# Optimization experiments

Hardware: AMD Instinct MI355X
Metric: run time of the kernel (lower is better)

## Reference

```python
import jax, jax.numpy as jnp
import numpy as np

K = 8        # fused SOS sections
C = 64       # channels (B*C after reshape)
T = 262144   # time samples (~6 s @ 44.1 kHz)


def setup_inputs() -> dict:
    key = jax.random.key(0)
    kx, kb, ka1, ka2 = jax.random.split(key, 4)
    x = jax.random.normal(kx, (C, T), dtype=jnp.float32)
    # Stable biquad coefficients: a0 = 1, |a1| < 0.5, |a2| < 0.4 keeps poles
    # strictly inside the unit circle (|a1| < 1 + a2 and |a2| < 1).
    b = jax.random.normal(kb, (K, 3), dtype=jnp.float32) * 0.3
    a1 = jax.random.uniform(ka1, (K, 1), minval=-0.5, maxval=0.5, dtype=jnp.float32)
    a2 = jax.random.uniform(ka2, (K, 1), minval=-0.4, maxval=0.4, dtype=jnp.float32)
    sos = jnp.concatenate([b, jnp.ones((K, 1), jnp.float32), a1, a2], axis=1)
    state_x = jnp.zeros((K, C, 2), jnp.float32)  # [x[n-1], x[n-2]] per section/channel
    state_y = jnp.zeros((K, C, 2), jnp.float32)  # [y[n-1], y[n-2]]
    return {"x": x, "sos": sos, "state_x": state_x, "state_y": state_y}


def _biquad_df1(x, b0, b1, b2, a1, a2, sx, sy):
    """Direct-form-1 biquad over time, vectorized across channels.

    x: [C, T]; sx, sy: [C, 2] holding (lag1, lag2). Returns y: [C, T].
    """
    def step(carry, xn):
        x1, x2, y1, y2 = carry
        yn = b0 * xn + b1 * x1 + b2 * x2 - a1 * y1 - a2 * y2
        return (xn, x1, yn, y1), yn

    init = (sx[:, 0], sx[:, 1], sy[:, 0], sy[:, 1])
    _, ys = jax.lax.scan(step, init, x.T)  # scan over T, carry [C]
    return ys.T


def reference(x, sos, state_x, state_y):
    # Serial cascade of K second-order sections (fallback path of forward()).
    out = x
    k = sos.shape[0]
    for s in range(k):
        out = _biquad_df1(out, sos[s, 0], sos[s, 1], sos[s, 2],
                          sos[s, 4], sos[s, 5], state_x[s], state_y[s])
    return out
```

## Files before the change

### kernel.cpp

```cpp
#include <hip/hip_runtime.h>

#define C 64
#define T 262144
#define K 8
#define L 256
#define W 192
#define B (T / L)
#define TT 64
#define OSTRIDE 65
#define TMAX (T - 16)

#define STEP(Y1, Y2, U1, U2, XIN)                                            \
  {                                                                          \
    float tkv[K];                                                            \
    tkv[0] = fmaf(b1c[0], U1,                                                \
             fmaf(b2c[0], U2, fmaf(na1[0], Y1[0], na2[0] * Y2[0])));         \
    _Pragma("unroll")                                                        \
    for (int k = 1; k < K; ++k)                                              \
      tkv[k] = fmaf(b1c[k], Y1[k - 1],                                       \
               fmaf(b2c[k], Y2[k - 1],                                       \
               fmaf(na1[k], Y1[k], na2[k] * Y2[k])));                        \
    float o = fmaf(b0c[0], (XIN), tkv[0]);                                   \
    U2 = (XIN);                                                              \
    _Pragma("unroll")                                                        \
    for (int k = 1; k < K; ++k) {                                            \
      float o2 = fmaf(b0c[k], o, tkv[k]);                                    \
      Y2[k - 1] = o;                                                         \
      o = o2;                                                                \
    }                                                                        \
    Y2[K - 1] = o;                                                           \
    lastout = o;                                                             \
  }

#define GROUP(XS, CBASE)                                                     \
  _Pragma("unroll")                                                          \
  for (int j = 0; j < 16; j += 2) {                                          \
    STEP(yA, yB, uA, uB, XS[j])                                              \
    orow[(CBASE) + j] = lastout;                                             \
    STEP(yB, yA, uB, uA, XS[j + 1])                                          \
    orow[(CBASE) + j + 1] = lastout;                                         \
  }

#define LOAD16(DST, PTR)                                                     \
  {                                                                          \
    const float4* p4_ = (const float4*)(PTR);                                \
    float4 q0_ = p4_[0], q1_ = p4_[1], q2_ = p4_[2], q3_ = p4_[3];           \
    DST[0] = q0_.x;  DST[1] = q0_.y;  DST[2] = q0_.z;  DST[3] = q0_.w;       \
    DST[4] = q1_.x;  DST[5] = q1_.y;  DST[6] = q1_.z;  DST[7] = q1_.w;       \
    DST[8] = q2_.x;  DST[9] = q2_.y;  DST[10] = q2_.z; DST[11] = q2_.w;      \
    DST[12] = q3_.x; DST[13] = q3_.y; DST[14] = q3_.z; DST[15] = q3_.w;      \
  }

__global__ __launch_bounds__(64) void sos_kernel(
    const float* __restrict__ x, const float* __restrict__ sos,
    const float* __restrict__ sx, const float* __restrict__ sy,
    float* __restrict__ out) {
  __shared__ float obuf[64 * OSTRIDE];

  const int h = blockIdx.x;
  const int b = (h & 7) * (B / 8) + (h >> 3);
  const int lane = threadIdx.x;

  float b0c[K], b1c[K], b2c[K], na1[K], na2[K];
#pragma unroll
  for (int k = 0; k < K; ++k) {
    b0c[k] = sos[k * 6 + 0];
    b1c[k] = sos[k * 6 + 1];
    b2c[k] = sos[k * 6 + 2];
    na1[k] = -sos[k * 6 + 4];
    na2[k] = -sos[k * 6 + 5];
  }

  const int t_out = b * L;
  const int tstart = (t_out >= W) ? (t_out - W) : 0;
  const int nch = (t_out + L - tstart) / TT;

  const float* xrow = x + (size_t)lane * T;
  float* orow = &obuf[lane * OSTRIDE];

  float yA[K], yB[K], uA, uB;
  if (tstart == 0) {
    uA = sx[lane * 2 + 0];
    uB = sx[lane * 2 + 1];
#pragma unroll
    for (int k = 0; k < K; ++k) {
      yA[k] = sy[(k * 64 + lane) * 2 + 0];
      yB[k] = sy[(k * 64 + lane) * 2 + 1];
    }
  } else {
    uA = xrow[tstart - 1];
    uB = xrow[tstart - 2];
#pragma unroll
    for (int k = 0; k < K; ++k) { yA[k] = 0.f; yB[k] = 0.f; }
  }

  float xA[16], xB[16], xC[16], xD[16];
  LOAD16(xA, xrow + tstart)
  LOAD16(xB, xrow + tstart + 16)

  float lastout = 0.f;
  for (int ch = 0; ch < nch; ++ch) {
    const int tc = tstart + ch * TT;

    LOAD16(xC, xrow + tc + 32)
    GROUP(xA, 0)
    LOAD16(xD, xrow + tc + 48)
    GROUP(xB, 16)
    { int tl = tc + 64;  if (tl > TMAX) tl = TMAX;
      LOAD16(xA, xrow + tl) }
    GROUP(xC, 32)
    { int tl = tc + 80;  if (tl > TMAX) tl = TMAX;
      LOAD16(xB, xrow + tl) }
    GROUP(xD, 48)

    if (tc >= t_out) {
      const int rr = lane >> 4;
      const int cc = (lane & 15) * 4;
#pragma unroll
      for (int it = 0; it < 16; ++it) {
        const int r = it * 4 + rr;
        float4 v;
        v.x = obuf[r * OSTRIDE + cc + 0];
        v.y = obuf[r * OSTRIDE + cc + 1];
        v.z = obuf[r * OSTRIDE + cc + 2];
        v.w = obuf[r * OSTRIDE + cc + 3];
        *reinterpret_cast<float4*>(&out[(size_t)r * T + tc + cc]) = v;
      }
    }
  }
  (void)lastout;
}

extern "C" void kernel_launch(void* const* d_in, const int* in_sizes, int n_in,
                              void* d_out, int out_size, void* d_ws,
                              size_t ws_size, hipStream_t stream) {
  const float* x = (const float*)d_in[0];
  const float* sos = (const float*)d_in[1];
  const float* sx = (const float*)d_in[2];
  const float* sy = (const float*)d_in[3];
  float* out = (float*)d_out;
  (void)d_ws;

  sos_kernel<<<B, 64, 0, stream>>>(x, sos, sx, sy, out);
}
```

Measured before the change: 137.1 us.

## Double-buffer full 64-sample chunks in registers to prefetch a whole chunk ahead

Replaces the rolling four-slice prefetch with two full register chunk buffers (p and q) that alternate, issuing all loads for the next 64-sample chunk before computing the current one, with a sched_barrier to keep them ordered. The loop is unrolled by two to swap buffers without copies. Launch bounds now request one wave per SIMD so the compiler may use more registers. The aim is to hide more global load latency behind the serial recurrence, at the cost of higher register pressure.

```diff
diff --git a/kernel.cpp b/kernel.cpp
--- a/kernel.cpp
+++ b/kernel.cpp
@@ -51,7 +51,39 @@
     DST[12] = q3_.x; DST[13] = q3_.y; DST[14] = q3_.z; DST[15] = q3_.w;      \
   }
 
-__global__ __launch_bounds__(64) void sos_kernel(
+#define PART(C0, C1, C2, C3, N0, N1, N2, N3, TC)                             \
+  {                                                                          \
+    const int tc_ = (TC);                                                    \
+    int t0_ = tc_ + 64;  if (t0_ > TMAX) t0_ = TMAX;                         \
+    int t1_ = tc_ + 80;  if (t1_ > TMAX) t1_ = TMAX;                         \
+    int t2_ = tc_ + 96;  if (t2_ > TMAX) t2_ = TMAX;                         \
+    int t3_ = tc_ + 112; if (t3_ > TMAX) t3_ = TMAX;                         \
+    LOAD16(N0, xrow + t0_)                                                   \
+    LOAD16(N1, xrow + t1_)                                                   \
+    LOAD16(N2, xrow + t2_)                                                   \
+    LOAD16(N3, xrow + t3_)                                                   \
+    __builtin_amdgcn_sched_barrier(0);                                       \
+    GROUP(C0, 0)                                                             \
+    GROUP(C1, 16)                                                            \
+    GROUP(C2, 32)                                                            \
+    GROUP(C3, 48)                                                            \
+    if (tc_ >= t_out) {                                                      \
+      const int rr = lane >> 4;                                              \
+      const int cc = (lane & 15) * 4;                                        \
+      _Pragma("unroll")                                                      \
+      for (int it = 0; it < 16; ++it) {                                      \
+        const int r = it * 4 + rr;                                           \
+        float4 v;                                                            \
+        v.x = obuf[r * OSTRIDE + cc + 0];                                    \
+        v.y = obuf[r * OSTRIDE + cc + 1];                                    \
+        v.z = obuf[r * OSTRIDE + cc + 2];                                    \
+        v.w = obuf[r * OSTRIDE + cc + 3];                                    \
+        *reinterpret_cast<float4*>(&out[(size_t)r * T + tc_ + cc]) = v;      \
+      }                                                                      \
+    }                                                                        \
+  }
+
+__global__ __launch_bounds__(64, 1) void sos_kernel(
     const float* __restrict__ x, const float* __restrict__ sos,
     const float* __restrict__ sx, const float* __restrict__ sy,
     float* __restrict__ out) {
@@ -94,38 +126,19 @@
     for (int k = 0; k < K; ++k) { yA[k] = 0.f; yB[k] = 0.f; }
   }
 
-  float xA[16], xB[16], xC[16], xD[16];
-  LOAD16(xA, xrow + tstart)
-  LOAD16(xB, xrow + tstart + 16)
+  float pA[16], pB[16], pC[16], pD[16];
+  float qA[16], qB[16], qC[16], qD[16];
+  LOAD16(pA, xrow + tstart)
+  LOAD16(pB, xrow + tstart + 16)
+  LOAD16(pC, xrow + tstart + 32)
+  LOAD16(pD, xrow + tstart + 48)
 
   float lastout = 0.f;
-  for (int ch = 0; ch < nch; ++ch) {
+  for (int ch = 0; ch < nch; ch += 2) {
     const int tc = tstart + ch * TT;
-
-    LOAD16(xC, xrow + tc + 32)
-    GROUP(xA, 0)
-    LOAD16(xD, xrow + tc + 48)
-    GROUP(xB, 16)
-    { int tl = tc + 64;  if (tl > TMAX) tl = TMAX;
-      LOAD16(xA, xrow + tl) }
-    GROUP(xC, 32)
-    { int tl = tc + 80;  if (tl > TMAX) tl = TMAX;
-      LOAD16(xB, xrow + tl) }
-    GROUP(xD, 48)
-
-    if (tc >= t_out) {
-      const int rr = lane >> 4;
-      const int cc = (lane & 15) * 4;
-#pragma unroll
-      for (int it = 0; it < 16; ++it) {
-        const int r = it * 4 + rr;
-        float4 v;
-        v.x = obuf[r * OSTRIDE + cc + 0];
-        v.y = obuf[r * OSTRIDE + cc + 1];
-        v.z = obuf[r * OSTRIDE + cc + 2];
-        v.w = obuf[r * OSTRIDE + cc + 3];
-        *reinterpret_cast<float4*>(&out[(size_t)r * T + tc + cc]) = v;
-      }
+    PART(pA, pB, pC, pD, qA, qB, qC, qD, tc)
+    if (ch + 1 < nch) {
+      PART(qA, qB, qC, qD, pA, pB, pC, pD, tc + TT)
     }
   }
   (void)lastout;
```

Result: slower. 144.6 us (+5.4%).

## Split SOS cascade across two wavefronts pipelined through shared memory

Applied to the files above, without the earlier changes.

Sections 0-3 and 4-7 now run on separate wavefronts of a 128-thread block. Wave 0 filters chunk p and writes the intermediate signal to a double-buffered LDS tile, while wave 1 filters chunk p-1 in place and writes the final output. The intent is to halve the serial dependency chain per wave and raise parallelism. In exchange it adds a __syncthreads per chunk, one extra pipeline stage, and warm-up state handling for the second half. The second half's warm-up starts from zero state at tstart, so accuracy depends on the W-sample warm-up being long enough for the intermediate signal.

```diff
diff --git a/kernel.cpp b/kernel.cpp
--- a/kernel.cpp
+++ b/kernel.cpp
@@ -3,42 +3,43 @@
 #define C 64
 #define T 262144
 #define K 8
+#define KH 4
 #define L 256
 #define W 192
 #define B (T / L)
 #define TT 64
-#define OSTRIDE 65
+#define STRIDE 65
 #define TMAX (T - 16)
 
-#define STEP(Y1, Y2, U1, U2, XIN)                                            \
+#define STEP4(Y1, Y2, U1, U2, XIN)                                           \
   {                                                                          \
-    float tkv[K];                                                            \
+    float tkv[KH];                                                           \
     tkv[0] = fmaf(b1c[0], U1,                                                \
              fmaf(b2c[0], U2, fmaf(na1[0], Y1[0], na2[0] * Y2[0])));         \
     _Pragma("unroll")                                                        \
-    for (int k = 1; k < K; ++k)                                              \
+    for (int k = 1; k < KH; ++k)                                             \
       tkv[k] = fmaf(b1c[k], Y1[k - 1],                                       \
                fmaf(b2c[k], Y2[k - 1],                                       \
                fmaf(na1[k], Y1[k], na2[k] * Y2[k])));                        \
     float o = fmaf(b0c[0], (XIN), tkv[0]);                                   \
     U2 = (XIN);                                                              \
     _Pragma("unroll")                                                        \
-    for (int k = 1; k < K; ++k) {                                            \
+    for (int k = 1; k < KH; ++k) {                                           \
       float o2 = fmaf(b0c[k], o, tkv[k]);                                    \
       Y2[k - 1] = o;                                                         \
       o = o2;                                                                \
     }                                                                        \
-    Y2[K - 1] = o;                                                           \
+    Y2[KH - 1] = o;                                                          \
     lastout = o;                                                             \
   }
 
-#define GROUP(XS, CBASE)                                                     \
+#define GROUP_W0(XS, ROW, CB)                                                \
   _Pragma("unroll")                                                          \
-  for (int j = 0; j < 16; j += 2) {                                          \
-    STEP(yA, yB, uA, uB, XS[j])                                              \
-    orow[(CBASE) + j] = lastout;                                             \
-    STEP(yB, yA, uB, uA, XS[j + 1])                                          \
-    orow[(CBASE) + j + 1] = lastout;                                         \
+  for (int jj = 0; jj < 16; jj += 2) {                                       \
+    STEP4(yA, yB, uA, uB, XS[jj])                                            \
+    (ROW)[(CB) + jj] = lastout;                                              \
+    STEP4(yB, yA, uB, uA, XS[jj + 1])                                        \
+    (ROW)[(CB) + jj + 1] = lastout;                                          \
   }
 
 #define LOAD16(DST, PTR)                                                     \
@@ -51,82 +52,129 @@
     DST[12] = q3_.x; DST[13] = q3_.y; DST[14] = q3_.z; DST[15] = q3_.w;      \
   }
 
-__global__ __launch_bounds__(64) void sos_kernel(
+__global__ __launch_bounds__(128) void sos_kernel(
     const float* __restrict__ x, const float* __restrict__ sos,
     const float* __restrict__ sx, const float* __restrict__ sy,
     float* __restrict__ out) {
-  __shared__ float obuf[64 * OSTRIDE];
+  __shared__ float hbuf[2][64 * STRIDE];
 
   const int h = blockIdx.x;
   const int b = (h & 7) * (B / 8) + (h >> 3);
-  const int lane = threadIdx.x;
+  const int wid = threadIdx.x >> 6;
+  const int lane = threadIdx.x & 63;
 
-  float b0c[K], b1c[K], b2c[K], na1[K], na2[K];
+  float b0c[KH], b1c[KH], b2c[KH], na1[KH], na2[KH];
 #pragma unroll
-  for (int k = 0; k < K; ++k) {
-    b0c[k] = sos[k * 6 + 0];
-    b1c[k] = sos[k * 6 + 1];
-    b2c[k] = sos[k * 6 + 2];
-    na1[k] = -sos[k * 6 + 4];
-    na2[k] = -sos[k * 6 + 5];
+  for (int k = 0; k < KH; ++k) {
+    const int kg = wid * KH + k;
+    b0c[k] = sos[kg * 6 + 0];
+    b1c[k] = sos[kg * 6 + 1];
+    b2c[k] = sos[kg * 6 + 2];
+    na1[k] = -sos[kg * 6 + 4];
+    na2[k] = -sos[kg * 6 + 5];
   }
 
   const int t_out = b * L;
   const int tstart = (t_out >= W) ? (t_out - W) : 0;
-  const int nch = (t_out + L - tstart) / TT;
+  const int nwarm = (t_out - tstart) / TT;
+  const int nch = nwarm + L / TT;
 
   const float* xrow = x + (size_t)lane * T;
-  float* orow = &obuf[lane * OSTRIDE];
 
-  float yA[K], yB[K], uA, uB;
+  float yA[KH], yB[KH], uA, uB;
   if (tstart == 0) {
-    uA = sx[lane * 2 + 0];
-    uB = sx[lane * 2 + 1];
+    uA = sx[(wid * 256 + lane) * 2 + 0];
+    uB = sx[(wid * 256 + lane) * 2 + 1];
 #pragma unroll
-    for (int k = 0; k < K; ++k) {
-      yA[k] = sy[(k * 64 + lane) * 2 + 0];
-      yB[k] = sy[(k * 64 + lane) * 2 + 1];
+    for (int k = 0; k < KH; ++k) {
+      const int kg = wid * KH + k;
+      yA[k] = sy[(kg * 64 + lane) * 2 + 0];
+      yB[k] = sy[(kg * 64 + lane) * 2 + 1];
     }
   } else {
-    uA = xrow[tstart - 1];
-    uB = xrow[tstart - 2];
+    if (wid == 0) {
+      uA = xrow[tstart - 1];
+      uB = xrow[tstart - 2];
+    } else {
+      uA = 0.f;
+      uB = 0.f;
+    }
 #pragma unroll
-    for (int k = 0; k < K; ++k) { yA[k] = 0.f; yB[k] = 0.f; }
+    for (int k = 0; k < KH; ++k) { yA[k] = 0.f; yB[k] = 0.f; }
   }
 
   float xA[16], xB[16], xC[16], xD[16];
-  LOAD16(xA, xrow + tstart)
-  LOAD16(xB, xrow + tstart + 16)
+  if (wid == 0) {
+    LOAD16(xA, xrow + tstart)
+    LOAD16(xB, xrow + tstart + 16)
+  }
 
   float lastout = 0.f;
-  for (int ch = 0; ch < nch; ++ch) {
-    const int tc = tstart + ch * TT;
-
-    LOAD16(xC, xrow + tc + 32)
-    GROUP(xA, 0)
-    LOAD16(xD, xrow + tc + 48)
-    GROUP(xB, 16)
-    { int tl = tc + 64;  if (tl > TMAX) tl = TMAX;
-      LOAD16(xA, xrow + tl) }
-    GROUP(xC, 32)
-    { int tl = tc + 80;  if (tl > TMAX) tl = TMAX;
-      LOAD16(xB, xrow + tl) }
-    GROUP(xD, 48)
-
-    if (tc >= t_out) {
-      const int rr = lane >> 4;
-      const int cc = (lane & 15) * 4;
+  for (int p = 0; p <= nch; ++p) {
+    if (wid == 0) {
+      if (p < nch) {
+        const int tc = tstart + p * TT;
+        float* myrow = &hbuf[p & 1][lane * STRIDE];
+        LOAD16(xC, xrow + tc + 32)
+        GROUP_W0(xA, myrow, 0)
+        LOAD16(xD, xrow + tc + 48)
+        GROUP_W0(xB, myrow, 16)
+        { int tl = tc + 64;  if (tl > TMAX) tl = TMAX;
+          LOAD16(xA, xrow + tl) }
+        GROUP_W0(xC, myrow, 32)
+        { int tl = tc + 80;  if (tl > TMAX) tl = TMAX;
+          LOAD16(xB, xrow + tl) }
+        GROUP_W0(xD, myrow, 48)
+      }
+    } else {
+      const int q = p - 1;
+      if (q >= 0) {
+        const int tq = tstart + q * TT;
+        float* myrow = &hbuf[q & 1][lane * STRIDE];
+        float xg0[8], xg1[8];
 #pragma unroll
-      for (int it = 0; it < 16; ++it) {
-        const int r = it * 4 + rr;
-        float4 v;
-        v.x = obuf[r * OSTRIDE + cc + 0];
-        v.y = obuf[r * OSTRIDE + cc + 1];
-        v.z = obuf[r * OSTRIDE + cc + 2];
-        v.w = obuf[r * OSTRIDE + cc + 3];
-        *reinterpret_cast<float4*>(&out[(size_t)r * T + tc + cc]) = v;
+        for (int j = 0; j < 8; ++j) xg0[j] = myrow[j];
+        for (int gg = 0; gg < 4; ++gg) {
+          const int tb = gg * 16;
+#pragma unroll
+          for (int j = 0; j < 8; ++j) xg1[j] = myrow[tb + 8 + j];
+#pragma unroll
+          for (int j = 0; j < 8; j += 2) {
+            STEP4(yA, yB, uA, uB, xg0[j])
+            myrow[tb + j] = lastout;
+            STEP4(yB, yA, uB, uA, xg0[j + 1])
+            myrow[tb + j + 1] = lastout;
+          }
+          if (gg + 1 < 4) {
+#pragma unroll
+            for (int j = 0; j < 8; ++j) xg0[j] = myrow[tb + 16 + j];
+          }
+#pragma unroll
+          for (int j = 0; j < 8; j += 2) {
+            STEP4(yA, yB, uA, uB, xg1[j])
+            myrow[tb + 8 + j] = lastout;
+            STEP4(yB, yA, uB, uA, xg1[j + 1])
+            myrow[tb + 8 + j + 1] = lastout;
+          }
+        }
+        if (q >= nwarm) {
+          const float* lbuf = hbuf[q & 1];
+          const int rr = lane >> 4;
+          const int cc = (lane & 15) * 4;
+#pragma unroll
+          for (int it = 0; it < 16; ++it) {
+            const int r = it * 4 + rr;
+            float4 v;
+            v.x = lbuf[r * STRIDE + cc + 0];
+            v.y = lbuf[r * STRIDE + cc + 1];
+            v.z = lbuf[r * STRIDE + cc + 2];
+            v.w = lbuf[r * STRIDE + cc + 3];
+            *reinterpret_cast<float4*>(&out[(size_t)r * T + tq + cc]) = v;
+          }
+        }
       }
     }
+    __syncthreads();
   }
   (void)lastout;
 }
@@ -141,5 +189,5 @@
   float* out = (float*)d_out;
   (void)d_ws;
 
-  sos_kernel<<<B, 64, 0, stream>>>(x, sos, sx, sy, out);
+  sos_kernel<<<B, 128, 0, stream>>>(x, sos, sx, sy, out);
 }
```

Result: no change. 134.9 us (-1.6%).
